# Kernel tuning notes

Hardware: AMD Instinct MI355X
Metric: run time of the kernel (lower is better)

## Reference

```python
import jax, jax.numpy as jnp
import numpy as np

B = 4096
INPUT_SIZE = 1024
HIDDEN_SIZE = 1024


def setup_inputs() -> dict:
    key = jax.random.key(0)
    ks = jax.random.split(key, 11)
    f32 = jnp.float32
    inp = {
        "x_t": jax.random.normal(ks[0], (B, INPUT_SIZE), dtype=f32),
        "h_prev": jax.random.normal(ks[1], (B, HIDDEN_SIZE), dtype=f32),
        "c_prev": jax.random.normal(ks[2], (B, HIDDEN_SIZE), dtype=f32),
        "W_f": jax.random.normal(ks[3], (INPUT_SIZE, HIDDEN_SIZE), dtype=f32),
        "W_i": jax.random.normal(ks[4], (INPUT_SIZE, HIDDEN_SIZE), dtype=f32),
        "W_c": jax.random.normal(ks[5], (INPUT_SIZE, HIDDEN_SIZE), dtype=f32),
        "W_o": jax.random.normal(ks[6], (INPUT_SIZE, HIDDEN_SIZE), dtype=f32),
        "U_f": jax.random.normal(ks[7], (HIDDEN_SIZE, HIDDEN_SIZE), dtype=f32),
        "U_i": jax.random.normal(ks[8], (HIDDEN_SIZE, HIDDEN_SIZE), dtype=f32),
        "U_c": jax.random.normal(ks[9], (HIDDEN_SIZE, HIDDEN_SIZE), dtype=f32),
        "U_o": jax.random.normal(ks[10], (HIDDEN_SIZE, HIDDEN_SIZE), dtype=f32),
        "b_f": jnp.zeros((HIDDEN_SIZE,), dtype=f32),
        "b_i": jnp.zeros((HIDDEN_SIZE,), dtype=f32),
        "b_c": jnp.zeros((HIDDEN_SIZE,), dtype=f32),
        "b_o": jnp.zeros((HIDDEN_SIZE,), dtype=f32),
    }
    return inp


def reference(x_t, h_prev, c_prev,
              W_f, W_i, W_c, W_o,
              U_f, U_i, U_c, U_o,
              b_f, b_i, b_c, b_o):
    # Fuse the 8 small GEMMs into 2 big ones by concatenating gate weights.
    W = jnp.concatenate([W_f, W_i, W_c, W_o], axis=1)  # [I, 4H]
    U = jnp.concatenate([U_f, U_i, U_c, U_o], axis=1)  # [H, 4H]
    b = jnp.concatenate([b_f, b_i, b_c, b_o], axis=0)  # [4H]
    gates = x_t @ W + h_prev @ U + b                    # [B, 4H]
    H = h_prev.shape[-1]
    f_t = jax.nn.sigmoid(gates[:, 0 * H:1 * H])
    i_t = jax.nn.sigmoid(gates[:, 1 * H:2 * H])
    c_tilda_t = jnp.tanh(gates[:, 2 * H:3 * H])
    o_t = jax.nn.sigmoid(gates[:, 3 * H:4 * H])
    c_t = f_t * c_prev + i_t * c_tilda_t
    h_t = o_t * jnp.tanh(c_t)
    return h_t
```

## Files before the change

### kernel.cpp

```cpp
#include <hip/hip_runtime.h>

typedef unsigned short u16;
typedef __attribute__((ext_vector_type(8))) short bf16x8;
typedef __attribute__((ext_vector_type(4))) float f32x4;

#define HID 1024
#define BATCH 4096
#define K3 6144
#define NGATE 4096
#define BK 32
#define NT 192

__device__ __forceinline__ u16 f2bf(float f) {
  unsigned int u = __float_as_uint(f);
  u += 0x7FFFu + ((u >> 16) & 1u);
  return (u16)(u >> 16);
}
__device__ __forceinline__ float bf2f(u16 h) {
  return __uint_as_float(((unsigned int)h) << 16);
}

__device__ __forceinline__ void load16_to_lds(const void* g, void* l) {
  __builtin_amdgcn_global_load_lds(
      (const __attribute__((address_space(1))) unsigned int*)g,
      (__attribute__((address_space(3))) unsigned int*)l, 16, 0, 0);
}

__device__ __forceinline__ float sigmoid_f(float x) {
  return 1.f / (1.f + __expf(-x));
}
__device__ __forceinline__ float tanh_f(float x) {
  return 1.f - 2.f / (__expf(2.f * x) + 1.f);
}

__global__ void pack_act(const float* __restrict__ x, const float* __restrict__ h,
                         u16* __restrict__ Bt) {
  size_t idx = (size_t)blockIdx.x * 256 + threadIdx.x;
  int m  = (int)(idx >> 9);
  int kq = (int)(idx & 511) << 2;
  const float* src = (kq < 1024) ? (x + (size_t)m * 1024 + kq)
                                 : (h + (size_t)m * 1024 + (kq - 1024));
  float4 v = *(const float4*)src;
  ushort4 hi, lo;
  hi.x = f2bf(v.x); lo.x = f2bf(v.x - bf2f(hi.x));
  hi.y = f2bf(v.y); lo.y = f2bf(v.y - bf2f(hi.y));
  hi.z = f2bf(v.z); lo.z = f2bf(v.z - bf2f(hi.z));
  hi.w = f2bf(v.w); lo.w = f2bf(v.w - bf2f(hi.w));
  u16* row = Bt + (size_t)m * K3;
  *(ushort4*)(row + kq)        = hi;
  *(ushort4*)(row + 2048 + kq) = lo;
  *(ushort4*)(row + 4096 + kq) = hi;
}

__global__ void pack_w(const float* __restrict__ Wf, const float* __restrict__ Wi,
                       const float* __restrict__ Wc, const float* __restrict__ Wo,
                       const float* __restrict__ Uf, const float* __restrict__ Ui,
                       const float* __restrict__ Uc, const float* __restrict__ Uo,
                       u16* __restrict__ P) {
  __shared__ float ldsT[32][33];
  int bid = blockIdx.x;
  int mat = bid >> 10;
  int tid = bid & 1023;
  int k0 = (tid >> 5) << 5;
  int h0 = (tid & 31) << 5;
  int g = mat & 3;
  const float* S;
  {
    const float* a = (mat & 1) ? ((mat & 2) ? Wo : Wi) : ((mat & 2) ? Wc : Wf);
    const float* b = (mat & 1) ? ((mat & 2) ? Uo : Ui) : ((mat & 2) ? Uc : Uf);
    S = (mat & 4) ? b : a;
  }
  int kbase = (mat & 4) ? 1024 : 0;

  int t = threadIdx.x;
  {
    int r0 = t >> 5;
    int c  = t & 31;
#pragma unroll
    for (int j = 0; j < 4; ++j)
      ldsT[c][r0 + 8 * j] = S[(size_t)(k0 + r0 + 8 * j) * 1024 + h0 + c];
  }
  __syncthreads();
  {
    int c  = t >> 3;
    int kq = (t & 7) << 2;
    int n  = ((h0 + c) << 2) + g;
    float v0 = ldsT[c][kq + 0], v1 = ldsT[c][kq + 1];
    float v2 = ldsT[c][kq + 2], v3 = ldsT[c][kq + 3];
    ushort4 hi, lo;
    hi.x = f2bf(v0); lo.x = f2bf(v0 - bf2f(hi.x));
    hi.y = f2bf(v1); lo.y = f2bf(v1 - bf2f(hi.y));
    hi.z = f2bf(v2); lo.z = f2bf(v2 - bf2f(hi.z));
    hi.w = f2bf(v3); lo.w = f2bf(v3 - bf2f(hi.w));
    u16* base = P + (size_t)n * K3 + kbase + k0 + kq;
    *(ushort4*)(base)        = hi;
    *(ushort4*)(base + 2048) = hi;
    *(ushort4*)(base + 4096) = lo;
  }
}

__global__ void pack_bias(const float* __restrict__ bf, const float* __restrict__ bi,
                          const float* __restrict__ bc, const float* __restrict__ bo,
                          float* __restrict__ bcat) {
  int i = blockIdx.x * 256 + threadIdx.x;
  if (i < NGATE) {
    int h = i >> 2, g = i & 3;
    const float* b = (g == 0) ? bf : (g == 1) ? bi : (g == 2) ? bc : bo;
    bcat[i] = b[h];
  }
}

__global__ __launch_bounds__(512, 2) void lstm_gemm(
    const u16* __restrict__ P, const u16* __restrict__ Bt,
    const float* __restrict__ bcat, const float* __restrict__ c_prev,
    float* __restrict__ out) {
  __shared__ __align__(16) u16 As[4][256 * BK];
  __shared__ __align__(16) u16 Bs[4][256 * BK];

  const int t = threadIdx.x;
  const int w = t >> 6;
  const int l = t & 63;

  const int bid = blockIdx.x;
  const int swz = ((bid & 7) << 5) + (bid >> 3);
  const int n0 = (swz & 15) << 8;
  const int m0 = (swz >> 4) << 8;

  const int wm = w >> 2;
  const int wn = w & 3;

  const int srow = t >> 2;
  const int ssl  = (((t & 3) ^ ((srow >> 1) & 3)) << 3);
  const u16* gA0 = P  + (size_t)(n0 + srow)       * K3 + ssl;
  const u16* gA1 = P  + (size_t)(n0 + 128 + srow) * K3 + ssl;
  const u16* gB0 = Bt + (size_t)(m0 + srow)       * K3 + ssl;
  const u16* gB1 = Bt + (size_t)(m0 + 128 + srow) * K3 + ssl;
  const int ldw0 = w << 9;
  const int ldw1 = 4096 + (w << 9);

  const int fr = l & 15;
  const int sl = l >> 4;
  int offA[8], offB[4];
#pragma unroll
  for (int i = 0; i < 8; ++i) {
    int ar = (wm << 7) + i * 16 + fr;
    offA[i] = ar * BK + ((sl ^ ((ar >> 1) & 3)) << 3);
  }
#pragma unroll
  for (int j = 0; j < 4; ++j) {
    int br = (wn << 6) + j * 16 + fr;
    offB[j] = br * BK + ((sl ^ ((br >> 1) & 3)) << 3);
  }

  f32x4 acc[8][4];
#pragma unroll
  for (int i = 0; i < 8; ++i)
#pragma unroll
    for (int j = 0; j < 4; ++j) acc[i][j] = (f32x4){0.f, 0.f, 0.f, 0.f};

#pragma unroll
  for (int pt = 0; pt < 3; ++pt) {
    const int kt = pt * BK;
    load16_to_lds(gA0 + kt, &As[pt][ldw0]);
    load16_to_lds(gA1 + kt, &As[pt][ldw1]);
    load16_to_lds(gB0 + kt, &Bs[pt][ldw0]);
    load16_to_lds(gB1 + kt, &Bs[pt][ldw1]);
  }
  asm volatile("s_waitcnt vmcnt(8)" ::: "memory");
  __builtin_amdgcn_s_barrier();

  for (int t4 = 0; t4 < NT; t4 += 4) {
#pragma unroll
    for (int u = 0; u < 4; ++u) {
      const int tt  = t4 + u;
      const int pfi = tt + 3;
      const int pkt = (pfi < NT ? pfi : NT - 1) * BK;
      const int pc  = (u + 3) & 3;

      bf16x8 aF[4], bF[4];
#pragma unroll
      for (int i = 0; i < 4; ++i) aF[i] = *(const bf16x8*)&As[u][offA[i]];
#pragma unroll
      for (int j = 0; j < 4; ++j) bF[j] = *(const bf16x8*)&Bs[u][offB[j]];
      load16_to_lds(gA0 + pkt, &As[pc][ldw0]);
      load16_to_lds(gA1 + pkt, &As[pc][ldw1]);
      __builtin_amdgcn_s_barrier();
      asm volatile("s_waitcnt lgkmcnt(0)" ::: "memory");
      __builtin_amdgcn_sched_barrier(0);
      __builtin_amdgcn_s_setprio(1);
#pragma unroll
      for (int i = 0; i < 4; ++i)
#pragma unroll
        for (int j = 0; j < 4; ++j)
          acc[i][j] = __builtin_amdgcn_mfma_f32_16x16x32_bf16(aF[i], bF[j], acc[i][j], 0, 0, 0);
      __builtin_amdgcn_s_setprio(0);
      __builtin_amdgcn_s_barrier();

      bf16x8 aG[4];
#pragma unroll
      for (int i = 0; i < 4; ++i) aG[i] = *(const bf16x8*)&As[u][offA[4 + i]];
      load16_to_lds(gB0 + pkt, &Bs[pc][ldw0]);
      load16_to_lds(gB1 + pkt, &Bs[pc][ldw1]);
      __builtin_amdgcn_s_barrier();
      asm volatile("s_waitcnt lgkmcnt(0)" ::: "memory");
      __builtin_amdgcn_sched_barrier(0);
      __builtin_amdgcn_s_setprio(1);
#pragma unroll
      for (int i = 0; i < 4; ++i)
#pragma unroll
        for (int j = 0; j < 4; ++j)
          acc[4 + i][j] = __builtin_amdgcn_mfma_f32_16x16x32_bf16(aG[i], bF[j], acc[4 + i][j], 0, 0, 0);
      __builtin_amdgcn_s_setprio(0);
      asm volatile("s_waitcnt vmcnt(8)" ::: "memory");
      __builtin_amdgcn_s_barrier();
    }
  }

  const int n_base = n0 + (wm << 7);
  const int m_base = m0 + (wn << 6);
#pragma unroll
  for (int i = 0; i < 8; ++i) {
    int nf = n_base + i * 16 + ((l >> 4) << 2);
    int hq = nf >> 2;
    float4 b4 = *(const float4*)&bcat[nf];
#pragma unroll
    for (int j = 0; j < 4; ++j) {
      int m = m_base + j * 16 + fr;
      f32x4 a = acc[i][j];
      float ft = sigmoid_f(a[0] + b4.x);
      float it = sigmoid_f(a[1] + b4.y);
      float ct = tanh_f   (a[2] + b4.z);
      float ot = sigmoid_f(a[3] + b4.w);
      float cp = c_prev[(size_t)m * HID + hq];
      float cn = ft * cp + it * ct;
      out[(size_t)m * HID + hq] = ot * tanh_f(cn);
    }
  }
}

extern "C" void kernel_launch(void* const* d_in, const int* in_sizes, int n_in,
                              void* d_out, int out_size, void* d_ws, size_t ws_size,
                              hipStream_t stream) {
  const float* x  = (const float*)d_in[0];
  const float* hp = (const float*)d_in[1];
  const float* cp = (const float*)d_in[2];
  const float* Wf = (const float*)d_in[3];
  const float* Wi = (const float*)d_in[4];
  const float* Wc = (const float*)d_in[5];
  const float* Wo = (const float*)d_in[6];
  const float* Uf = (const float*)d_in[7];
  const float* Ui = (const float*)d_in[8];
  const float* Uc = (const float*)d_in[9];
  const float* Uo = (const float*)d_in[10];
  const float* bf = (const float*)d_in[11];
  const float* bi = (const float*)d_in[12];
  const float* bc = (const float*)d_in[13];
  const float* bo = (const float*)d_in[14];

  const size_t P_BYTES  = (size_t)NGATE * K3 * 2;
  const size_t BT_BYTES = (size_t)BATCH * K3 * 2;
  u16*   Pw   = (u16*)d_ws;
  u16*   Bt   = (u16*)((char*)d_ws + P_BYTES);
  float* bcat = (float*)((char*)d_ws + P_BYTES + BT_BYTES);
  float* out  = (float*)d_out;

  pack_act <<<dim3(8192), dim3(256), 0, stream>>>(x, hp, Bt);
  pack_w   <<<dim3(8192), dim3(256), 0, stream>>>(Wf, Wi, Wc, Wo, Uf, Ui, Uc, Uo, Pw);
  pack_bias<<<dim3(16),   dim3(256), 0, stream>>>(bf, bi, bc, bo, bcat);
  lstm_gemm<<<dim3(256),  dim3(512), 0, stream>>>(Pw, Bt, bcat, cp, out);
}
```

Baseline: 222.1 us.

## Restructure GEMM pipeline to double-buffered BK=64 tiles split into halves

```diff
diff --git a/kernel.cpp b/kernel.cpp
--- a/kernel.cpp
+++ b/kernel.cpp
@@ -8,8 +8,8 @@
 #define BATCH 4096
 #define K3 6144
 #define NGATE 4096
-#define BK 32
-#define NT 192
+#define BK 64
+#define NT 96
 
 __device__ __forceinline__ u16 f2bf(float f) {
   unsigned int u = __float_as_uint(f);
@@ -114,8 +114,8 @@
     const u16* __restrict__ P, const u16* __restrict__ Bt,
     const float* __restrict__ bcat, const float* __restrict__ c_prev,
     float* __restrict__ out) {
-  __shared__ __align__(16) u16 As[4][256 * BK];
-  __shared__ __align__(16) u16 Bs[4][256 * BK];
+  __shared__ __align__(16) u16 As[2][2][8192];
+  __shared__ __align__(16) u16 Bs[2][2][8192];
 
   const int t = threadIdx.x;
   const int w = t >> 6;
@@ -129,14 +129,11 @@
   const int wm = w >> 2;
   const int wn = w & 3;
 
-  const int srow = t >> 2;
-  const int ssl  = (((t & 3) ^ ((srow >> 1) & 3)) << 3);
-  const u16* gA0 = P  + (size_t)(n0 + srow)       * K3 + ssl;
-  const u16* gA1 = P  + (size_t)(n0 + 128 + srow) * K3 + ssl;
-  const u16* gB0 = Bt + (size_t)(m0 + srow)       * K3 + ssl;
-  const u16* gB1 = Bt + (size_t)(m0 + 128 + srow) * K3 + ssl;
-  const int ldw0 = w << 9;
-  const int ldw1 = 4096 + (w << 9);
+  const int srow = (w << 4) + (l >> 2);
+  const int ssl  = (((l & 3) ^ ((l >> 3) & 3)) << 3);
+  const u16* gA = P  + (size_t)(n0 + srow) * K3 + ssl;
+  const u16* gB = Bt + (size_t)(m0 + srow) * K3 + ssl;
+  const int dq = w << 9;
 
   const int fr = l & 15;
   const int sl = l >> 4;
@@ -144,12 +141,12 @@
 #pragma unroll
   for (int i = 0; i < 8; ++i) {
     int ar = (wm << 7) + i * 16 + fr;
-    offA[i] = ar * BK + ((sl ^ ((ar >> 1) & 3)) << 3);
+    offA[i] = ar * 32 + ((sl ^ ((ar >> 1) & 3)) << 3);
   }
 #pragma unroll
   for (int j = 0; j < 4; ++j) {
     int br = (wn << 6) + j * 16 + fr;
-    offB[j] = br * BK + ((sl ^ ((br >> 1) & 3)) << 3);
+    offB[j] = br * 32 + ((sl ^ ((br >> 1) & 3)) << 3);
   }
 
   f32x4 acc[8][4];
@@ -158,63 +155,96 @@
 #pragma unroll
     for (int j = 0; j < 4; ++j) acc[i][j] = (f32x4){0.f, 0.f, 0.f, 0.f};
 
-#pragma unroll
-  for (int pt = 0; pt < 3; ++pt) {
-    const int kt = pt * BK;
-    load16_to_lds(gA0 + kt, &As[pt][ldw0]);
-    load16_to_lds(gA1 + kt, &As[pt][ldw1]);
-    load16_to_lds(gB0 + kt, &Bs[pt][ldw0]);
-    load16_to_lds(gB1 + kt, &Bs[pt][ldw1]);
-  }
-  asm volatile("s_waitcnt vmcnt(8)" ::: "memory");
+  load16_to_lds(gA,                            &As[0][0][dq]);
+  load16_to_lds(gA + (size_t)128 * K3,         &As[0][0][dq + 4096]);
+  load16_to_lds(gB,                            &Bs[0][0][dq]);
+  load16_to_lds(gB + (size_t)128 * K3,         &Bs[0][0][dq + 4096]);
+  load16_to_lds(gA + 32,                       &As[0][1][dq]);
+  load16_to_lds(gA + 32 + (size_t)128 * K3,    &As[0][1][dq + 4096]);
+  load16_to_lds(gB + 32,                       &Bs[0][1][dq]);
+  load16_to_lds(gB + 32 + (size_t)128 * K3,    &Bs[0][1][dq + 4096]);
+  asm volatile("s_waitcnt vmcnt(4)" ::: "memory");
   __builtin_amdgcn_s_barrier();
 
-  for (int t4 = 0; t4 < NT; t4 += 4) {
-#pragma unroll
-    for (int u = 0; u < 4; ++u) {
-      const int tt  = t4 + u;
-      const int pfi = tt + 3;
-      const int pkt = (pfi < NT ? pfi : NT - 1) * BK;
-      const int pc  = (u + 3) & 3;
-
-      bf16x8 aF[4], bF[4];
-#pragma unroll
-      for (int i = 0; i < 4; ++i) aF[i] = *(const bf16x8*)&As[u][offA[i]];
-#pragma unroll
-      for (int j = 0; j < 4; ++j) bF[j] = *(const bf16x8*)&Bs[u][offB[j]];
-      load16_to_lds(gA0 + pkt, &As[pc][ldw0]);
-      load16_to_lds(gA1 + pkt, &As[pc][ldw1]);
-      __builtin_amdgcn_s_barrier();
-      asm volatile("s_waitcnt lgkmcnt(0)" ::: "memory");
-      __builtin_amdgcn_sched_barrier(0);
-      __builtin_amdgcn_s_setprio(1);
-#pragma unroll
-      for (int i = 0; i < 4; ++i)
-#pragma unroll
-        for (int j = 0; j < 4; ++j)
-          acc[i][j] = __builtin_amdgcn_mfma_f32_16x16x32_bf16(aF[i], bF[j], acc[i][j], 0, 0, 0);
-      __builtin_amdgcn_s_setprio(0);
-      __builtin_amdgcn_s_barrier();
-
-      bf16x8 aG[4];
-#pragma unroll
-      for (int i = 0; i < 4; ++i) aG[i] = *(const bf16x8*)&As[u][offA[4 + i]];
-      load16_to_lds(gB0 + pkt, &Bs[pc][ldw0]);
-      load16_to_lds(gB1 + pkt, &Bs[pc][ldw1]);
-      __builtin_amdgcn_s_barrier();
-      asm volatile("s_waitcnt lgkmcnt(0)" ::: "memory");
-      __builtin_amdgcn_sched_barrier(0);
-      __builtin_amdgcn_s_setprio(1);
-#pragma unroll
-      for (int i = 0; i < 4; ++i)
-#pragma unroll
-        for (int j = 0; j < 4; ++j)
-          acc[4 + i][j] = __builtin_amdgcn_mfma_f32_16x16x32_bf16(aG[i], bF[j], acc[4 + i][j], 0, 0, 0);
-      __builtin_amdgcn_s_setprio(0);
-      asm volatile("s_waitcnt vmcnt(8)" ::: "memory");
-      __builtin_amdgcn_s_barrier();
-    }
-  }
+  bf16x8 aF[4], aG[4], bF[4];
+
+#define PH_OPEN                                                                 \
+    __builtin_amdgcn_s_barrier();                                               \
+    asm volatile("s_waitcnt lgkmcnt(0)" ::: "memory");                          \
+    __builtin_amdgcn_sched_barrier(0);                                          \
+    __builtin_amdgcn_s_setprio(1);
+
+#define PH_CLOSE                                                                \
+    __builtin_amdgcn_s_setprio(0);                                              \
+    __builtin_amdgcn_s_barrier();
+
+#define PH_CLOSE_VM                                                             \
+    __builtin_amdgcn_s_setprio(0);                                              \
+    asm volatile("s_waitcnt vmcnt(4)" ::: "memory");                            \
+    __builtin_amdgcn_s_barrier();
+
+#define MFMA16(IB, AOP)                                                         \
+  _Pragma("unroll")                                                             \
+  for (int i = 0; i < 4; ++i)                                                   \
+    _Pragma("unroll")                                                           \
+    for (int j = 0; j < 4; ++j)                                                 \
+      acc[(IB) + i][j] = __builtin_amdgcn_mfma_f32_16x16x32_bf16(               \
+          AOP[i], bF[j], acc[(IB) + i][j], 0, 0, 0);
+
+#define TILE_BODY(BUF, TT)                                                      \
+  {                                                                             \
+    const int pf = ((TT) + 1 < NT) ? (TT) + 1 : NT - 1;                         \
+    const size_t pfk = (size_t)pf * BK;                                         \
+    const int BN_ = (BUF) ^ 1;                                                  \
+                                     \
+    _Pragma("unroll")                                                           \
+    for (int i = 0; i < 4; ++i) aF[i] = *(const bf16x8*)&As[BUF][0][offA[i]];   \
+    _Pragma("unroll")                                                           \
+    for (int j = 0; j < 4; ++j) bF[j] = *(const bf16x8*)&Bs[BUF][0][offB[j]];   \
+    load16_to_lds(gA + pfk,                    &As[BN_][0][dq]);                \
+    load16_to_lds(gA + pfk + (size_t)128 * K3, &As[BN_][0][dq + 4096]);         \
+    PH_OPEN                                                                     \
+    MFMA16(0, aF)                                                               \
+    PH_CLOSE                                                                    \
+                         \
+    _Pragma("unroll")                                                           \
+    for (int i = 0; i < 4; ++i) aG[i] = *(const bf16x8*)&As[BUF][0][offA[4+i]]; \
+    load16_to_lds(gB + pfk,                    &Bs[BN_][0][dq]);                \
+    load16_to_lds(gB + pfk + (size_t)128 * K3, &Bs[BN_][0][dq + 4096]);         \
+    PH_OPEN                                                                     \
+    MFMA16(4, aG)                                                               \
+    PH_CLOSE_VM                             \
+                                     \
+    _Pragma("unroll")                                                           \
+    for (int i = 0; i < 4; ++i) aF[i] = *(const bf16x8*)&As[BUF][1][offA[i]];   \
+    _Pragma("unroll")                                                           \
+    for (int j = 0; j < 4; ++j) bF[j] = *(const bf16x8*)&Bs[BUF][1][offB[j]];   \
+    load16_to_lds(gA + pfk + 32,                    &As[BN_][1][dq]);           \
+    load16_to_lds(gA + pfk + 32 + (size_t)128 * K3, &As[BN_][1][dq + 4096]);    \
+    PH_OPEN                                                                     \
+    MFMA16(0, aF)                                                               \
+    PH_CLOSE                                                                    \
+                                     \
+    _Pragma("unroll")                                                           \
+    for (int i = 0; i < 4; ++i) aG[i] = *(const bf16x8*)&As[BUF][1][offA[4+i]]; \
+    load16_to_lds(gB + pfk + 32,                    &Bs[BN_][1][dq]);           \
+    load16_to_lds(gB + pfk + 32 + (size_t)128 * K3, &Bs[BN_][1][dq + 4096]);    \
+    PH_OPEN                                                                     \
+    MFMA16(4, aG)                                                               \
+    PH_CLOSE_VM                      \
+  }
+
+  for (int T = 0; T < NT; T += 2) {
+    TILE_BODY(0, T)
+    TILE_BODY(1, T + 1)
+  }
+#undef TILE_BODY
+#undef MFMA16
+#undef PH_OPEN
+#undef PH_CLOSE
+#undef PH_CLOSE_VM
+
+  asm volatile("s_waitcnt vmcnt(0)" ::: "memory");
 
   const int n_base = n0 + (wm << 7);
   const int m_base = m0 + (wn << 6);
```

New measurement: 228.0 us. 1.03x slower.
